# Kernel tuning notes

Hardware: AMD Instinct MI355X
Metric: run time of the kernel (lower is better)

The kernel has to match this reference:

```python
import jax, jax.numpy as jnp
import numpy as np

REEIG_EPS = 1e-4  # standard SPDNet ReEig rectification threshold


def _bimap(X, W):
    # X: [B, C, n, n] SPD, W: [C, n, m] semi-orthogonal -> W^T X W : [B, C, m, m]
    return jnp.einsum('cik,bcij,cjl->bckl', W, X, W)


def _reeig(X):
    # Eigen-rectification: clamp eigenvalues at REEIG_EPS, reconstruct.
    w, U = jnp.linalg.eigh(X)
    w = jnp.maximum(w, REEIG_EPS)
    return jnp.einsum('bcik,bck,bcjk->bcij', U, w, U)


def _logeig(X):
    # Matrix log via eigendecomposition (eigenvalues > 0 after ReEig).
    w, U = jnp.linalg.eigh(X)
    return jnp.einsum('bcik,bck,bcjk->bcij', U, jnp.log(w), U)


def setup_inputs() -> dict:
    key = jax.random.key(0)
    k_x, k_w1, k_w2, k_wl, k_bl = jax.random.split(key, 5)
    B, n1, n2, n_cls = 131072, 12, 11, 52
    # Build SPD inputs: A A^T / n + eps I
    A = jax.random.normal(k_x, (B, 1, n1, n1), dtype=jnp.float32)
    x = jnp.einsum('bcij,bckj->bcik', A, A) / n1 + 1e-3 * jnp.eye(n1, dtype=jnp.float32)
    # Stiefel (semi-orthogonal) BiMap weights, as in SPDNet
    Q1 = jnp.linalg.qr(jax.random.normal(k_w1, (n1, n1), dtype=jnp.float32))[0]
    w1 = Q1[None, :, :]                      # [1, 12, 12]
    Q2 = jnp.linalg.qr(jax.random.normal(k_w2, (n1, n1), dtype=jnp.float32))[0]
    w2 = Q2[:, :n2][None, :, :]              # [1, 12, 11]
    w_lin = jax.random.normal(k_wl, (n_cls, n2 * n2), dtype=jnp.float32) * (1.0 / np.sqrt(n2 * n2))
    b_lin = jnp.zeros((n_cls,), dtype=jnp.float32)
    return {"x": x, "w1": w1, "w2": w2, "w_lin": w_lin, "b_lin": b_lin}


def reference(x, w1, w2, w_lin, b_lin):
    h = _reeig(_bimap(x, w1))                # [B,1,12,12]
    h = _reeig(_bimap(h, w2))                # [B,1,11,11]
    h = _logeig(h).reshape(x.shape[0], -1)   # [B,121]
    return h @ w_lin.T + b_lin               # [B,52]
```

## Files before the change

### kernel.cpp

```cpp
#include <hip/hip_runtime.h>
#include <math.h>


#define NSWEEP 5

#define WS_V 0
#define WS_B 160
#define WS_W 256

typedef float v2f __attribute__((ext_vector_type(2)));

__device__ __forceinline__ v2f fma2(v2f a, v2f b, v2f c) {
  return __builtin_elementwise_fma(a, b, c);
}
__device__ __forceinline__ v2f sp2(float x) {
  v2f r; r.x = x; r.y = x; return r;
}

__device__ __forceinline__ constexpr int UT(int i, int j) {
  return i * 11 - (i * (i - 1)) / 2 + (j - i);
}

template <int P, int Q>
__device__ __forceinline__ void csCompute(const float (&M)[66], float& c, float& s,
                                          float& t) {
  const float app = M[UT(P, P)], aqq = M[UT(Q, Q)], apq = M[UT(P, Q)];
  const float d2 = aqq - app;
  const float a2 = apq + apq;
  const float r = __builtin_amdgcn_sqrtf(
      __builtin_fmaf(d2, d2, __builtin_fmaf(a2, a2, 1e-60f)));
  const float den = d2 + __builtin_copysignf(r, d2);
  t = a2 * __builtin_amdgcn_rcpf(den);
  c = __builtin_amdgcn_rsqf(__builtin_fmaf(t, t, 1.0f));
  s = t * c;
}

template <int P, int Q>
__device__ __forceinline__ void applyRot(float (&M)[66], v2f (&U2)[66], float c,
                                         float s, float t) {
  const float apq = M[UT(P, Q)];
#pragma unroll
  for (int k = 0; k < 11; ++k) {
    if (k == P || k == Q) continue;
    const int ikp = (k < P) ? UT(k, P) : UT(P, k);
    const int ikq = (k < Q) ? UT(k, Q) : UT(Q, k);
    const float akp = M[ikp], akq = M[ikq];
    M[ikp] = __builtin_fmaf(c, akp, -s * akq);
    M[ikq] = __builtin_fmaf(s, akp, c * akq);
  }
  M[UT(P, P)] = __builtin_fmaf(-t, apq, M[UT(P, P)]);
  M[UT(Q, Q)] = __builtin_fmaf(t, apq, M[UT(Q, Q)]);
  M[UT(P, Q)] = 0.0f;
  const v2f c2 = sp2(c), s2 = sp2(s);
#pragma unroll
  for (int r2 = 0; r2 < 6; ++r2) {
    const v2f up = U2[P * 6 + r2], uq = U2[Q * 6 + r2];
    U2[P * 6 + r2] = fma2(c2, up, -(s2 * uq));
    U2[Q * 6 + r2] = fma2(s2, up, c2 * uq);
  }
}

template <int R, int K>
struct PairRR {
  static constexpr int A0 = (R + K) % 11;
  static constexpr int B0 = (R + 11 - K) % 11;
  static constexpr int P = A0 < B0 ? A0 : B0;
  static constexpr int Q = A0 < B0 ? B0 : A0;
};

template <int R>
__device__ __forceinline__ void jround(float (&M)[66], v2f (&U2)[66]) {
  float c1, s1, t1, c2, s2, t2, c3, s3, t3, c4, s4, t4, c5, s5, t5;
  csCompute<PairRR<R, 1>::P, PairRR<R, 1>::Q>(M, c1, s1, t1);
  csCompute<PairRR<R, 2>::P, PairRR<R, 2>::Q>(M, c2, s2, t2);
  csCompute<PairRR<R, 3>::P, PairRR<R, 3>::Q>(M, c3, s3, t3);
  csCompute<PairRR<R, 4>::P, PairRR<R, 4>::Q>(M, c4, s4, t4);
  csCompute<PairRR<R, 5>::P, PairRR<R, 5>::Q>(M, c5, s5, t5);
  applyRot<PairRR<R, 1>::P, PairRR<R, 1>::Q>(M, U2, c1, s1, t1);
  applyRot<PairRR<R, 2>::P, PairRR<R, 2>::Q>(M, U2, c2, s2, t2);
  applyRot<PairRR<R, 3>::P, PairRR<R, 3>::Q>(M, U2, c3, s3, t3);
  applyRot<PairRR<R, 4>::P, PairRR<R, 4>::Q>(M, U2, c4, s4, t4);
  applyRot<PairRR<R, 5>::P, PairRR<R, 5>::Q>(M, U2, c5, s5, t5);
}

template <int R>
struct RoundSeq {
  static __device__ __forceinline__ void run(float (&M)[66], v2f (&U2)[66]) {
    jround<R>(M, U2);
    if constexpr (R < 10) RoundSeq<R + 1>::run(M, U2);
  }
};

__global__ __launch_bounds__(256) void prep_kernel(
    const float* __restrict__ w1, const float* __restrict__ w2,
    const float* __restrict__ wlin, const float* __restrict__ blin,
    float* __restrict__ ws) {
  const int g = blockIdx.x * 256 + threadIdx.x;
  const int gs = gridDim.x * 256;
  for (int idx = g; idx < 144; idx += gs) {
    const int i = idx / 12, l = idx % 12;
    float acc = 0.f;
    if (l < 11) {
#pragma unroll
      for (int j = 0; j < 12; ++j) acc = __builtin_fmaf(w1[i * 12 + j], w2[j * 11 + l], acc);
    }
    ws[WS_V + idx] = acc;
  }
  for (int idx = g; idx < 52; idx += gs) ws[WS_B + idx] = blin[idx];
  for (int idx = g; idx < 52 * 68; idx += gs) {
    const int c = idx / 68, t = idx % 68;
    float v = 0.f;
    if (t < 66) {
      int i = 0, rem = t;
      while (rem >= 11 - i) { rem -= 11 - i; ++i; }
      const int j = i + rem;
      v = wlin[c * 121 + i * 11 + j];
      if (i != j) v += wlin[c * 121 + j * 11 + i];
    }
    ws[WS_W + idx] = v;
  }
}

__global__ __attribute__((amdgpu_flat_work_group_size(256, 256)))
__attribute__((amdgpu_waves_per_eu(1, 1)))
void manifold_kernel(const float* __restrict__ x, const float* __restrict__ ws,
                     float* __restrict__ out, int B) {
  __shared__ __align__(16) float sV[12 * 12];
  const int tid = threadIdx.x;
  if (tid < 36) {
    reinterpret_cast<float4*>(sV)[tid] =
        reinterpret_cast<const float4*>(ws + WS_V)[tid];
  }
  __syncthreads();

  const int b = blockIdx.x * 256 + tid;
  if (b >= B) return;

  float M[66];
#pragma unroll
  for (int e = 0; e < 66; ++e) M[e] = 0.f;
  const float4* xb4 = reinterpret_cast<const float4*>(x + (size_t)b * 144);
#pragma unroll 1
  for (int ib = 0; ib < 3; ++ib) {
    float xr[4][12];
#pragma unroll
    for (int r = 0; r < 4; ++r) {
      const float4 a0 = xb4[(ib * 4 + r) * 3 + 0];
      const float4 a1 = xb4[(ib * 4 + r) * 3 + 1];
      const float4 a2 = xb4[(ib * 4 + r) * 3 + 2];
      xr[r][0] = a0.x; xr[r][1] = a0.y; xr[r][2] = a0.z; xr[r][3] = a0.w;
      xr[r][4] = a1.x; xr[r][5] = a1.y; xr[r][6] = a1.z; xr[r][7] = a1.w;
      xr[r][8] = a2.x; xr[r][9] = a2.y; xr[r][10] = a2.z; xr[r][11] = a2.w;
    }
    v2f w2[4][6];
#pragma unroll
    for (int r = 0; r < 4; ++r)
#pragma unroll
      for (int l2 = 0; l2 < 6; ++l2) { w2[r][l2].x = 0.f; w2[r][l2].y = 0.f; }
#pragma unroll
    for (int j = 0; j < 12; ++j) {
      v2f vj[6];
      {
        const float4 v0 = *reinterpret_cast<const float4*>(&sV[j * 12 + 0]);
        const float4 v1 = *reinterpret_cast<const float4*>(&sV[j * 12 + 4]);
        const float4 v2 = *reinterpret_cast<const float4*>(&sV[j * 12 + 8]);
        vj[0].x = v0.x; vj[0].y = v0.y; vj[1].x = v0.z; vj[1].y = v0.w;
        vj[2].x = v1.x; vj[2].y = v1.y; vj[3].x = v1.z; vj[3].y = v1.w;
        vj[4].x = v2.x; vj[4].y = v2.y; vj[5].x = v2.z; vj[5].y = v2.w;
      }
#pragma unroll
      for (int r = 0; r < 4; ++r) {
        const v2f xb = sp2(xr[r][j]);
#pragma unroll
        for (int l2 = 0; l2 < 6; ++l2) w2[r][l2] = fma2(xb, vj[l2], w2[r][l2]);
      }
    }
#pragma unroll
    for (int r = 0; r < 4; ++r) {
      const int i = ib * 4 + r;
      const float4 u0 = *reinterpret_cast<const float4*>(&sV[i * 12 + 0]);
      const float4 u1 = *reinterpret_cast<const float4*>(&sV[i * 12 + 4]);
      const float4 u2 = *reinterpret_cast<const float4*>(&sV[i * 12 + 8]);
      const float ui[11] = {u0.x, u0.y, u0.z, u0.w, u1.x, u1.y, u1.z, u1.w,
                            u2.x, u2.y, u2.z};
      float wv[11];
#pragma unroll
      for (int l = 0; l < 11; ++l)
        wv[l] = (l & 1) ? w2[r][l >> 1].y : w2[r][l >> 1].x;
#pragma unroll
      for (int k = 0; k < 11; ++k)
#pragma unroll
        for (int l = k; l < 11; ++l)
          M[UT(k, l)] = __builtin_fmaf(ui[k], wv[l], M[UT(k, l)]);
    }
  }

  v2f U2[66];
#pragma unroll
  for (int e = 0; e < 66; ++e) { U2[e].x = 0.f; U2[e].y = 0.f; }
#pragma unroll
  for (int d = 0; d < 11; ++d) {
    if (d & 1) U2[d * 6 + (d >> 1)].y = 1.f;
    else       U2[d * 6 + (d >> 1)].x = 1.f;
  }
#pragma unroll 1
  for (int sweep = 0; sweep < NSWEEP; ++sweep) {
    RoundSeq<0>::run(M, U2);
  }

  float lw[11];
#pragma unroll
  for (int k = 0; k < 11; ++k) lw[k] = __logf(fmaxf(M[UT(k, k)], 1e-4f));

  v2f L2[33];
#pragma unroll
  for (int i = 0; i < 11; ++i) {
    float tk[11];
#pragma unroll
    for (int k = 0; k < 11; ++k) {
      const v2f u = U2[k * 6 + (i >> 1)];
      const float uik = (i & 1) ? u.y : u.x;
      tk[k] = lw[k] * uik;
    }
#pragma unroll
    for (int j = i; j < 11; ++j) {
      float acc = 0.f;
#pragma unroll
      for (int k = 0; k < 11; ++k) {
        const v2f u = U2[k * 6 + (j >> 1)];
        const float ujk = (j & 1) ? u.y : u.x;
        acc = __builtin_fmaf(tk[k], ujk, acc);
      }
      const int idx = UT(i, j);
      if (idx & 1) L2[idx >> 1].y = acc;
      else         L2[idx >> 1].x = acc;
    }
  }

  const float* __restrict__ wsym = ws + WS_W;
  const float* __restrict__ bl = ws + WS_B;
  float* ob = out + (size_t)b * 52;
#pragma unroll 1
  for (int c4 = 0; c4 < 13; ++c4) {
    float ov[4];
#pragma unroll
    for (int cc = 0; cc < 4; ++cc) {
      const int c = c4 * 4 + cc;
      const v2f* __restrict__ wr2 = reinterpret_cast<const v2f*>(wsym + c * 68);
      v2f a0 = sp2(0.f), a1 = sp2(0.f), a2 = sp2(0.f);
#pragma unroll
      for (int t = 0; t < 30; t += 3) {
        a0 = fma2(wr2[t + 0], L2[t + 0], a0);
        a1 = fma2(wr2[t + 1], L2[t + 1], a1);
        a2 = fma2(wr2[t + 2], L2[t + 2], a2);
      }
      a0 = fma2(wr2[30], L2[30], a0);
      a1 = fma2(wr2[31], L2[31], a1);
      a2 = fma2(wr2[32], L2[32], a2);
      const v2f sum = (a0 + a1) + a2;
      ov[cc] = bl[c] + (sum.x + sum.y);
    }
    float4 o;
    o.x = ov[0]; o.y = ov[1]; o.z = ov[2]; o.w = ov[3];
    reinterpret_cast<float4*>(ob)[c4] = o;
  }
}

extern "C" void kernel_launch(void* const* d_in, const int* in_sizes, int n_in,
                              void* d_out, int out_size, void* d_ws, size_t ws_size,
                              hipStream_t stream) {
  const float* x = (const float*)d_in[0];
  const float* w1 = (const float*)d_in[1];
  const float* w2 = (const float*)d_in[2];
  const float* wlin = (const float*)d_in[3];
  const float* blin = (const float*)d_in[4];
  float* out = (float*)d_out;
  float* ws = (float*)d_ws;
  const int B = in_sizes[0] / 144;
  hipLaunchKernelGGL(prep_kernel, dim3(8), dim3(256), 0, stream,
                     w1, w2, wlin, blin, ws);
  const int grid = (B + 255) / 256;
  hipLaunchKernelGGL(manifold_kernel, dim3(grid), dim3(256), 0, stream,
                     x, ws, out, B);
}
```

Before: 267.9 us.

## Use fast-Givens scaled rotations in the Jacobi eigensolver

```diff
diff --git a/kernel.cpp b/kernel.cpp
--- a/kernel.cpp
+++ b/kernel.cpp
@@ -22,22 +22,30 @@
 }
 
 template <int P, int Q>
-__device__ __forceinline__ void csCompute(const float (&M)[66], float& c, float& s,
-                                          float& t) {
-  const float app = M[UT(P, P)], aqq = M[UT(Q, Q)], apq = M[UT(P, Q)];
+__device__ __forceinline__ void csComputeFG(const float (&M)[66], float (&d)[11],
+                                            float& al, float& be, float& o) {
+  const float dp = d[P], dq = d[Q];
+  const float rp = dp * dp, rq = dq * dq;
+  const float app = rp * M[UT(P, P)];
+  const float aqq = rq * M[UT(Q, Q)];
+  const float apq = (dp * dq) * M[UT(P, Q)];
   const float d2 = aqq - app;
   const float a2 = apq + apq;
   const float r = __builtin_amdgcn_sqrtf(
       __builtin_fmaf(d2, d2, __builtin_fmaf(a2, a2, 1e-60f)));
   const float den = d2 + __builtin_copysignf(r, d2);
-  t = a2 * __builtin_amdgcn_rcpf(den);
-  c = __builtin_amdgcn_rsqf(__builtin_fmaf(t, t, 1.0f));
-  s = t * c;
+  const float t = a2 * __builtin_amdgcn_rcpf(den);
+  o = __builtin_fmaf(t, t, 1.0f);
+  const float c = __builtin_amdgcn_rsqf(o);
+  al = t * (dq * __builtin_amdgcn_rcpf(dp));
+  be = t * (dp * __builtin_amdgcn_rcpf(dq));
+  d[P] = c * dp;
+  d[Q] = c * dq;
 }
 
 template <int P, int Q>
-__device__ __forceinline__ void applyRot(float (&M)[66], v2f (&U2)[66], float c,
-                                         float s, float t) {
+__device__ __forceinline__ void applyRotFG(float (&M)[66], v2f (&U2)[66],
+                                           float al, float be, float o) {
   const float apq = M[UT(P, Q)];
 #pragma unroll
   for (int k = 0; k < 11; ++k) {
@@ -45,18 +53,18 @@
     const int ikp = (k < P) ? UT(k, P) : UT(P, k);
     const int ikq = (k < Q) ? UT(k, Q) : UT(Q, k);
     const float akp = M[ikp], akq = M[ikq];
-    M[ikp] = __builtin_fmaf(c, akp, -s * akq);
-    M[ikq] = __builtin_fmaf(s, akp, c * akq);
-  }
-  M[UT(P, P)] = __builtin_fmaf(-t, apq, M[UT(P, P)]);
-  M[UT(Q, Q)] = __builtin_fmaf(t, apq, M[UT(Q, Q)]);
+    M[ikp] = __builtin_fmaf(-al, akq, akp);
+    M[ikq] = __builtin_fmaf(be, akp, akq);
+  }
+  M[UT(P, P)] = o * __builtin_fmaf(-al, apq, M[UT(P, P)]);
+  M[UT(Q, Q)] = o * __builtin_fmaf(be, apq, M[UT(Q, Q)]);
   M[UT(P, Q)] = 0.0f;
-  const v2f c2 = sp2(c), s2 = sp2(s);
+  const v2f a2v = sp2(al), b2v = sp2(be);
 #pragma unroll
   for (int r2 = 0; r2 < 6; ++r2) {
     const v2f up = U2[P * 6 + r2], uq = U2[Q * 6 + r2];
-    U2[P * 6 + r2] = fma2(c2, up, -(s2 * uq));
-    U2[Q * 6 + r2] = fma2(s2, up, c2 * uq);
+    U2[P * 6 + r2] = fma2(-a2v, uq, up);
+    U2[Q * 6 + r2] = fma2(b2v, up, uq);
   }
 }
 
@@ -69,25 +77,27 @@
 };
 
 template <int R>
-__device__ __forceinline__ void jround(float (&M)[66], v2f (&U2)[66]) {
-  float c1, s1, t1, c2, s2, t2, c3, s3, t3, c4, s4, t4, c5, s5, t5;
-  csCompute<PairRR<R, 1>::P, PairRR<R, 1>::Q>(M, c1, s1, t1);
-  csCompute<PairRR<R, 2>::P, PairRR<R, 2>::Q>(M, c2, s2, t2);
-  csCompute<PairRR<R, 3>::P, PairRR<R, 3>::Q>(M, c3, s3, t3);
-  csCompute<PairRR<R, 4>::P, PairRR<R, 4>::Q>(M, c4, s4, t4);
-  csCompute<PairRR<R, 5>::P, PairRR<R, 5>::Q>(M, c5, s5, t5);
-  applyRot<PairRR<R, 1>::P, PairRR<R, 1>::Q>(M, U2, c1, s1, t1);
-  applyRot<PairRR<R, 2>::P, PairRR<R, 2>::Q>(M, U2, c2, s2, t2);
-  applyRot<PairRR<R, 3>::P, PairRR<R, 3>::Q>(M, U2, c3, s3, t3);
-  applyRot<PairRR<R, 4>::P, PairRR<R, 4>::Q>(M, U2, c4, s4, t4);
-  applyRot<PairRR<R, 5>::P, PairRR<R, 5>::Q>(M, U2, c5, s5, t5);
+__device__ __forceinline__ void jround(float (&M)[66], v2f (&U2)[66],
+                                       float (&d)[11]) {
+  float a1, b1, o1, a2, b2, o2, a3, b3, o3, a4, b4, o4, a5, b5, o5;
+  csComputeFG<PairRR<R, 1>::P, PairRR<R, 1>::Q>(M, d, a1, b1, o1);
+  csComputeFG<PairRR<R, 2>::P, PairRR<R, 2>::Q>(M, d, a2, b2, o2);
+  csComputeFG<PairRR<R, 3>::P, PairRR<R, 3>::Q>(M, d, a3, b3, o3);
+  csComputeFG<PairRR<R, 4>::P, PairRR<R, 4>::Q>(M, d, a4, b4, o4);
+  csComputeFG<PairRR<R, 5>::P, PairRR<R, 5>::Q>(M, d, a5, b5, o5);
+  applyRotFG<PairRR<R, 1>::P, PairRR<R, 1>::Q>(M, U2, a1, b1, o1);
+  applyRotFG<PairRR<R, 2>::P, PairRR<R, 2>::Q>(M, U2, a2, b2, o2);
+  applyRotFG<PairRR<R, 3>::P, PairRR<R, 3>::Q>(M, U2, a3, b3, o3);
+  applyRotFG<PairRR<R, 4>::P, PairRR<R, 4>::Q>(M, U2, a4, b4, o4);
+  applyRotFG<PairRR<R, 5>::P, PairRR<R, 5>::Q>(M, U2, a5, b5, o5);
 }
 
 template <int R>
 struct RoundSeq {
-  static __device__ __forceinline__ void run(float (&M)[66], v2f (&U2)[66]) {
-    jround<R>(M, U2);
-    if constexpr (R < 10) RoundSeq<R + 1>::run(M, U2);
+  static __device__ __forceinline__ void run(float (&M)[66], v2f (&U2)[66],
+                                             float (&d)[11]) {
+    jround<R>(M, U2, d);
+    if constexpr (R < 10) RoundSeq<R + 1>::run(M, U2, d);
   }
 };
 
@@ -199,18 +209,25 @@
 #pragma unroll
   for (int e = 0; e < 66; ++e) { U2[e].x = 0.f; U2[e].y = 0.f; }
 #pragma unroll
-  for (int d = 0; d < 11; ++d) {
-    if (d & 1) U2[d * 6 + (d >> 1)].y = 1.f;
-    else       U2[d * 6 + (d >> 1)].x = 1.f;
-  }
+  for (int d0 = 0; d0 < 11; ++d0) {
+    if (d0 & 1) U2[d0 * 6 + (d0 >> 1)].y = 1.f;
+    else        U2[d0 * 6 + (d0 >> 1)].x = 1.f;
+  }
+  float d[11];
+#pragma unroll
+  for (int k = 0; k < 11; ++k) d[k] = 1.f;
 #pragma unroll 1
   for (int sweep = 0; sweep < NSWEEP; ++sweep) {
-    RoundSeq<0>::run(M, U2);
-  }
-
-  float lw[11];
-#pragma unroll
-  for (int k = 0; k < 11; ++k) lw[k] = __logf(fmaxf(M[UT(k, k)], 1e-4f));
+    RoundSeq<0>::run(M, U2, d);
+  }
+
+  float g[11];
+#pragma unroll
+  for (int k = 0; k < 11; ++k) {
+    const float rk = d[k] * d[k];
+    const float lwk = __logf(fmaxf(rk * M[UT(k, k)], 1e-4f));
+    g[k] = lwk * rk;
+  }
 
   v2f L2[33];
 #pragma unroll
@@ -220,7 +237,7 @@
     for (int k = 0; k < 11; ++k) {
       const v2f u = U2[k * 6 + (i >> 1)];
       const float uik = (i & 1) ? u.y : u.x;
-      tk[k] = lw[k] * uik;
+      tk[k] = g[k] * uik;
     }
 #pragma unroll
     for (int j = i; j < 11; ++j) {
```

After: 271.6 us. Within noise of the previous version (+1.4%).
